# Kernel optimization log

Measured on AMD Instinct MI355X. Metric: run time of the kernel, lower is better.

## Reference

```python
import jax, jax.numpy as jnp
import numpy as np

N_HEAD, D_HEAD, EMBED = 16, 64, 1024
B, Q_LEN, MEM_LEN = 2, 1024, 1024
K_LEN = Q_LEN + MEM_LEN  # == r_len
LN_EPS = 1e-3  # keras LayerNormalization default


def rel_shift(x):
    # x: [B, H, q, r]  (Transformer-XL relative shift)
    b, h, q, r = x.shape
    x = jnp.pad(x, ((0, 0), (0, 0), (0, 0), (1, 0)))
    x = x.reshape(b, h, r + 1, q)[:, :, 1:, :]
    return x.reshape(b, h, q, r)


def setup_inputs() -> dict:
    key = jax.random.key(0)
    ks = jax.random.split(key, 12)
    s = 0.02
    w = jax.random.normal(ks[0], (B, Q_LEN, EMBED), jnp.float32)
    r = jax.random.normal(ks[1], (K_LEN, EMBED), jnp.float32)
    member = jax.random.normal(ks[2], (B, MEM_LEN, EMBED), jnp.float32)
    r_w_bias = jax.random.normal(ks[3], (N_HEAD, D_HEAD), jnp.float32) * s
    r_r_bias = jax.random.normal(ks[4], (N_HEAD, D_HEAD), jnp.float32) * s
    # causal mask over [q_len, k_len]: position i may attend to mem + keys <= mem_len+i
    qi = jnp.arange(Q_LEN)[:, None]
    kj = jnp.arange(K_LEN)[None, :]
    attn_mask = (kj > qi + MEM_LEN).astype(jnp.float32)
    Wq = jax.random.normal(ks[5], (EMBED, N_HEAD * D_HEAD), jnp.float32) * s
    Wk = jax.random.normal(ks[6], (EMBED, N_HEAD * D_HEAD), jnp.float32) * s
    Wv = jax.random.normal(ks[7], (EMBED, N_HEAD * D_HEAD), jnp.float32) * s
    Wr = jax.random.normal(ks[8], (EMBED, N_HEAD * D_HEAD), jnp.float32) * s
    Wo = jax.random.normal(ks[9], (N_HEAD * D_HEAD, EMBED), jnp.float32) * s
    ln_gamma = jnp.ones((EMBED,), jnp.float32)
    ln_beta = jnp.zeros((EMBED,), jnp.float32)
    return {"w": w, "r": r, "attn_mask": attn_mask, "r_w_bias": r_w_bias,
            "r_r_bias": r_r_bias, "member": member, "Wq": Wq, "Wk": Wk,
            "Wv": Wv, "Wr": Wr, "Wo": Wo, "ln_gamma": ln_gamma, "ln_beta": ln_beta}


def reference(w, r, attn_mask, r_w_bias, r_r_bias, member, Wq, Wk, Wv, Wr, Wo, ln_gamma, ln_beta):
    b, q_len, _ = w.shape
    cat = jnp.concatenate([member, w], axis=1)          # [B, klen, D]
    klen = cat.shape[1]
    q = (cat @ Wq)[:, -q_len:].reshape(b, q_len, N_HEAD, D_HEAD)
    k = (cat @ Wk).reshape(b, klen, N_HEAD, D_HEAD)
    v = (cat @ Wv).reshape(b, klen, N_HEAD, D_HEAD)
    rr = (r @ Wr).reshape(r.shape[0], N_HEAD, D_HEAD)    # [rlen, H, dh]
    rw_q = q + r_w_bias[None, None]                      # content bias
    rr_q = q + r_r_bias[None, None]                      # position bias
    AC = jnp.einsum('bqhd,bkhd->bhqk', rw_q, k)
    BD = jnp.einsum('bqhd,rhd->bhqr', rr_q, rr)
    BD = rel_shift(BD)
    attn = (AC + BD) / jnp.sqrt(jnp.float32(EMBED))      # note: sqrt(embed), as in source
    m = attn_mask[None, None]                            # [1,1,q,k]
    attn = attn * (1.0 - m) - 1e30 * m
    score = jax.nn.softmax(attn, axis=-1)
    out = jnp.einsum('bhqk,bkhd->bqhd', score, v).reshape(b, q_len, N_HEAD * D_HEAD)
    out = out @ Wo
    x = w + out
    mu = jnp.mean(x, axis=-1, keepdims=True)
    var = jnp.mean(jnp.square(x - mu), axis=-1, keepdims=True)
    return (x - mu) * jax.lax.rsqrt(var + LN_EPS) * ln_gamma + ln_beta
```

## Files before the change

kernel.cpp:

```cpp
#include <hip/hip_runtime.h>


typedef __bf16 bf16;
typedef __bf16 bf16x4 __attribute__((ext_vector_type(4)));
typedef __bf16 bf16x8 __attribute__((ext_vector_type(8)));
typedef float f32x4 __attribute__((ext_vector_type(4)));

#define MFMA16(a, b, c) __builtin_amdgcn_mfma_f32_16x16x32_bf16((a), (b), (c), 0, 0, 0)

constexpr int E = 1024;
constexpr int NH = 16;
constexpr int DH = 64;
constexpr int QL = 1024;
constexpr int ML = 1024;
constexpr int KLEN = 2048;

__device__ __forceinline__ void ldg2lds16(const bf16* g, bf16* l) {
    __builtin_amdgcn_global_load_lds(
        (const __attribute__((address_space(1))) unsigned int*)g,
        (__attribute__((address_space(3))) unsigned int*)l, 16, 0, 0);
}

__device__ __forceinline__ bf16x8 frag8(const bf16* t, int row, int ch) {
    return *(const bf16x8*)(t + row * 64 + ((ch ^ (row & 7)) << 3));
}

__global__ void pre_k(const float* __restrict__ Wq, const float* __restrict__ Wk,
                      const float* __restrict__ Wv, const float* __restrict__ Wr,
                      const float* __restrict__ Wo, const float* __restrict__ member,
                      const float* __restrict__ w, bf16* __restrict__ WqT,
                      bf16* __restrict__ WkT, bf16* __restrict__ WvT,
                      bf16* __restrict__ WrT, bf16* __restrict__ WoT,
                      bf16* __restrict__ cat) {
    const int id = blockIdx.x;
    const int tid = threadIdx.x;
    __shared__ float t[32][33];
    if (id < 5120) {
        const float* W; bf16* WT;
        switch (id >> 10) {
            case 0: W = Wq; WT = WqT; break;
            case 1: W = Wk; WT = WkT; break;
            case 2: W = Wv; WT = WvT; break;
            case 3: W = Wr; WT = WrT; break;
            default: W = Wo; WT = WoT; break;
        }
        int xy = id & 1023;
        int bx = (xy & 31) * 32, by = (xy >> 5) * 32;
        int x = tid & 31, y = tid >> 5;
        for (int yy = y; yy < 32; yy += 8)
            t[yy][x] = W[(by + yy) * E + bx + x];
        __syncthreads();
        for (int yy = y; yy < 32; yy += 8)
            WT[(bx + yy) * E + by + x] = (bf16)t[x][yy];
    } else {
        int row = id - 5120;
        int b = row >> 11, jj = row & 2047;
        const float* src = (jj < ML) ? member + ((size_t)(b * ML + jj)) * E
                                     : w + ((size_t)(b * QL + (jj - ML))) * E;
        float4 f = *(const float4*)(src + tid * 4);
        bf16x4 o;
        o[0] = (bf16)f.x; o[1] = (bf16)f.y; o[2] = (bf16)f.z; o[3] = (bf16)f.w;
        *(bf16x4*)(cat + (size_t)row * E + tid * 4) = o;
    }
}

__global__ __launch_bounds__(256) void proj_k(
    const bf16* __restrict__ cat, const float* __restrict__ r,
    const bf16* __restrict__ WqT, const bf16* __restrict__ WkT,
    const bf16* __restrict__ WvT, const bf16* __restrict__ WrT,
    const float* __restrict__ rwb, const float* __restrict__ rrb,
    bf16* __restrict__ Qw, bf16* __restrict__ Qr, bf16* __restrict__ Kh,
    bf16* __restrict__ Vt, bf16* __restrict__ RRh) {
    __shared__ __align__(16) bf16 As[128 * 64];
    __shared__ __align__(16) bf16 Bs[128 * 64];
    const int tid = threadIdx.x;
    const int wave = tid >> 6, lane = tid & 63, quad = lane >> 4, l16 = lane & 15;

    int id = blockIdx.x, zone, base;
    if (id < 128) { zone = 0; base = 0; }
    else if (id < 384) { zone = 1; base = 128; }
    else if (id < 640) { zone = 2; base = 384; }
    else { zone = 3; base = 640; }
    const int lid = id - base;
    const int bn = (lid & 7) * 128, bm = (lid >> 3) * 128;
    const bf16* Bt = (zone == 0) ? WqT : (zone == 1) ? WkT : (zone == 2) ? WvT : WrT;
    const int wm = (wave >> 1) * 64, wn = (wave & 1) * 64;

    f32x4 acc[4][4] = {};

    for (int kk = 0; kk < E; kk += 64) {
        if (zone == 3) {
            int srw = tid >> 3, cch = tid & 7;
            for (int c = 0; c < 4; ++c) {
                int row = c * 32 + srw;
                const float* ap = r + (size_t)(bm + row) * E + kk + cch * 8;
                float4 f0 = *(const float4*)ap;
                float4 f1 = *(const float4*)(ap + 4);
                bf16x8 v;
                v[0] = (bf16)f0.x; v[1] = (bf16)f0.y; v[2] = (bf16)f0.z; v[3] = (bf16)f0.w;
                v[4] = (bf16)f1.x; v[5] = (bf16)f1.y; v[6] = (bf16)f1.z; v[7] = (bf16)f1.w;
                *(bf16x8*)(As + row * 64 + ((cch ^ (row & 7)) << 3)) = v;
            }
        } else {
            for (int issue = 0; issue < 4; ++issue) {
                int q = (issue * 4 + wave) * 64 + lane;
                int row = q >> 3, cs = (q & 7) ^ ((q >> 3) & 7);
                int gm = bm + row;
                const bf16* ap;
                if (zone == 0) {
                    int b = gm >> 10;
                    ap = cat + ((size_t)(b * 2048 + 1024 + (gm & 1023))) * E;
                } else {
                    ap = cat + (size_t)gm * E;
                }
                ldg2lds16(ap + kk + cs * 8, As + (issue * 4 + wave) * 512);
            }
        }
        for (int issue = 0; issue < 4; ++issue) {
            int q = (issue * 4 + wave) * 64 + lane;
            int row = q >> 3, cs = (q & 7) ^ ((q >> 3) & 7);
            ldg2lds16(Bt + (size_t)(bn + row) * E + kk + cs * 8,
                      Bs + (issue * 4 + wave) * 512);
        }
        __syncthreads();
        for (int ks = 0; ks < 64; ks += 32) {
            bf16x8 af[4], bfr[4];
            for (int mt = 0; mt < 4; ++mt)
                af[mt] = frag8(As, wm + mt * 16 + l16, (ks >> 3) + quad);
            for (int nt = 0; nt < 4; ++nt)
                bfr[nt] = frag8(Bs, wn + nt * 16 + l16, (ks >> 3) + quad);
            for (int mt = 0; mt < 4; ++mt)
                for (int nt = 0; nt < 4; ++nt)
                    acc[mt][nt] = MFMA16(af[mt], bfr[nt], acc[mt][nt]);
        }
        __syncthreads();
    }

    if (zone == 2) {
        bf16* buf = ((wave < 2) ? As : Bs) + (wave & 1) * 4096;
        for (int mt = 0; mt < 4; ++mt)
            for (int nt = 0; nt < 4; ++nt)
                for (int rr = 0; rr < 4; ++rr) {
                    int lr = mt * 16 + quad * 4 + rr;
                    int lc = nt * 16 + l16;
                    buf[lr * 64 + (((lc >> 3) ^ (lr & 7)) << 3) + (lc & 7)] =
                        (bf16)acc[mt][nt][rr];
                }
        int h = (bn + wn) >> 6;
        int gmw = bm + wm;
        int b = gmw >> 11, jb = gmw & 2047;
        for (int dp = 0; dp < 8; ++dp) {
            int dl = dp * 8 + (lane >> 3);
            int jl = (lane & 7) * 8;
            bf16x8 tmp;
            for (int jj = 0; jj < 8; ++jj) {
                int rw = jl + jj;
                tmp[jj] = buf[rw * 64 + (((dl >> 3) ^ (rw & 7)) << 3) + (dl & 7)];
            }
            *(bf16x8*)(Vt + (((size_t)(b * NH + h) * DH + dl) * KLEN) + jb + jl) = tmp;
        }
        return;
    }

    for (int mt = 0; mt < 4; ++mt)
        for (int nt = 0; nt < 4; ++nt)
            for (int rr = 0; rr < 4; ++rr) {
                int row = bm + wm + mt * 16 + quad * 4 + rr;
                int col = bn + wn + nt * 16 + l16;
                float v = acc[mt][nt][rr];
                if (zone == 0) {
                    int b = row >> 10, i = row & 1023;
                    int h = col >> 6, d = col & 63;
                    size_t o = (((size_t)(b * NH + h) * QL) + i) * DH + d;
                    Qw[o] = (bf16)((v + rwb[col]) * 0.03125f);
                    Qr[o] = (bf16)((v + rrb[col]) * 0.03125f);
                } else if (zone == 1) {
                    int b = row >> 11, j = row & 2047;
                    int h = col >> 6, d = col & 63;
                    Kh[(((size_t)(b * NH + h) * KLEN) + j) * DH + d] = (bf16)v;
                } else {
                    int h = col >> 6, d = col & 63;
                    RRh[(((size_t)h * KLEN) + row) * DH + d] = (bf16)v;
                }
            }
}

__global__ __launch_bounds__(256) void attn_k(
    const bf16* __restrict__ Qw, const bf16* __restrict__ Qr,
    const bf16* __restrict__ Kh, const bf16* __restrict__ Vt,
    const bf16* __restrict__ RRh, bf16* __restrict__ AttO) {
    __shared__ __align__(16) bf16 Ks[2][64 * 64];
    __shared__ __align__(16) bf16 Vs[2][64 * 64];
    __shared__ __align__(16) bf16 RRing[3][64 * 64];
    __shared__ __align__(16) bf16 UB[4][16 * 88];

    const int tid = threadIdx.x;
    const int wave = tid >> 6, lane = tid & 63, quad = lane >> 4, l16 = lane & 15;
    const int id = blockIdx.x;
    const int b = id >> 8, h = (id >> 4) & 15;
    const int qt = (id < 256) ? (id & 15) : (15 - (id & 15));
    const int i0 = qt * 64;

    const bf16* Qwb = Qw + ((size_t)(b * NH + h) * QL) * DH;
    const bf16* Qrb = Qr + ((size_t)(b * NH + h) * QL) * DH;
    const bf16* Kb = Kh + ((size_t)(b * NH + h) * KLEN) * DH;
    const bf16* Vb = Vt + ((size_t)(b * NH + h) * DH) * KLEN;
    const bf16* Rb = RRh + ((size_t)h * KLEN) * DH;

    bf16x8 qw0, qw1, qr0, qr1;
    {
        int i = i0 + wave * 16 + l16;
        qw0 = *(const bf16x8*)(Qwb + (size_t)i * DH + quad * 8);
        qw1 = *(const bf16x8*)(Qwb + (size_t)i * DH + 32 + quad * 8);
        qr0 = *(const bf16x8*)(Qrb + (size_t)i * DH + quad * 8);
        qr1 = *(const bf16x8*)(Qrb + (size_t)i * DH + 32 + quad * 8);
    }

    float lpart[4] = {0.f, 0.f, 0.f, 0.f};
    f32x4 oacc[4] = {};

    const int ntiles = qt + 17;
    const int cbase = 15 - qt;
    const int ptbase = 3 - wave;

    auto stage_kv = [&](int t) {
        const int j0 = t * 64;
        bf16* Kd = Ks[t & 1];
        bf16* Vd = Vs[t & 1];
        for (int issue = 0; issue < 2; ++issue) {
            int q = (issue * 4 + wave) * 64 + lane;
            int row = q >> 3, cs = (q & 7) ^ ((q >> 3) & 7);
            ldg2lds16(Kb + (size_t)(j0 + row) * DH + cs * 8,
                      Kd + (issue * 4 + wave) * 512);
            ldg2lds16(Vb + (size_t)row * KLEN + j0 + cs * 8,
                      Vd + (issue * 4 + wave) * 512);
        }
    };
    auto stage_rr = [&](int c) {
        bf16* Rd = RRing[c % 3];
        for (int issue = 0; issue < 2; ++issue) {
            int q = (issue * 4 + wave) * 64 + lane;
            int row = q >> 3, cs = (q & 7) ^ ((q >> 3) & 7);
            int pr = c * 64 + row;
            pr = pr > KLEN - 1 ? KLEN - 1 : pr;
            ldg2lds16(Rb + (size_t)pr * DH + cs * 8, Rd + (issue * 4 + wave) * 512);
        }
    };

    stage_kv(0);
    stage_rr(cbase);
    stage_rr(cbase + 1);
    __syncthreads();

    for (int t = 0; t < ntiles; ++t) {
        const bf16* Kt = Ks[t & 1];
        const bf16* Vl = Vs[t & 1];
        const bf16* Rlo = RRing[(cbase + t) % 3];
        const bf16* Rhi = RRing[(cbase + t + 1) % 3];
        if (t + 1 < ntiles) {
            stage_kv(t + 1);
            stage_rr(cbase + t + 2);
        }

        f32x4 bacc[5];
        for (int pi = 0; pi < 5; ++pi) {
            int pt = ptbase + pi;
            const bf16* Rsrc = (pt < 4) ? Rlo : Rhi;
            int rrow = (pt & 3) * 16 + l16;
            f32x4 a = {};
            a = MFMA16(qr0, frag8(Rsrc, rrow, quad), a);
            a = MFMA16(qr1, frag8(Rsrc, rrow, 4 + quad), a);
            bacc[pi] = a;
        }

        f32x4 sacc[4];
        for (int nt = 0; nt < 4; ++nt) {
            f32x4 a = {};
            a = MFMA16(qw0, frag8(Kt, nt * 16 + l16, quad), a);
            a = MFMA16(qw1, frag8(Kt, nt * 16 + l16, 4 + quad), a);
            sacc[nt] = a;
        }

        float sv[4][4];
        const bool lastt = (t == ntiles - 1);
        for (int rr = 0; rr < 4; ++rr) {
            const int lr = quad * 4 + rr;
            const int srcl = quad * 16 + ((l16 - lr - 1) & 15);
            float g[5];
            for (int pi = 0; pi < 5; ++pi) g[pi] = __shfl(bacc[pi][rr], srcl);
            const bool hi = (l16 > lr);
            for (int nt = 0; nt < 4; ++nt) {
                float bdv = hi ? g[nt + 1] : g[nt];
                float p = __expf(sacc[nt][rr] + bdv);
                if (lastt) {
                    int i = i0 + wave * 16 + lr;
                    int j = t * 64 + nt * 16 + l16;
                    if (j > i + ML) p = 0.f;
                }
                sv[nt][rr] = p;
                lpart[rr] += p;
            }
        }

        for (int nt = 0; nt < 4; ++nt)
            for (int rr = 0; rr < 4; ++rr)
                UB[wave][(quad * 4 + rr) * 88 + nt * 16 + l16] = (bf16)sv[nt][rr];

        for (int c = 0; c < 2; ++c) {
            bf16x8 pa = *(const bf16x8*)(&UB[wave][l16 * 88 + c * 32 + quad * 8]);
            for (int nt = 0; nt < 4; ++nt) {
                bf16x8 vb = frag8(Vl, nt * 16 + l16, c * 4 + quad);
                oacc[nt] = MFMA16(pa, vb, oacc[nt]);
            }
        }
        __syncthreads();
    }

    float linv[4];
    for (int rr = 0; rr < 4; ++rr) {
        float v = lpart[rr];
        v += __shfl_xor(v, 1);
        v += __shfl_xor(v, 2);
        v += __shfl_xor(v, 4);
        v += __shfl_xor(v, 8);
        linv[rr] = 1.f / v;
    }

    for (int nt = 0; nt < 4; ++nt)
        for (int rr = 0; rr < 4; ++rr) {
            int i = i0 + wave * 16 + quad * 4 + rr;
            int d = nt * 16 + l16;
            AttO[((size_t)(b * QL + i)) * E + h * DH + d] =
                (bf16)(oacc[nt][rr] * linv[rr]);
        }
}

__global__ __launch_bounds__(256) void gemm_o(
    const bf16* __restrict__ A, const bf16* __restrict__ Bt,
    float* __restrict__ Xp) {
    __shared__ __align__(16) bf16 As[128 * 64];
    __shared__ __align__(16) bf16 Bs[128 * 64];
    const int tid = threadIdx.x;
    const int wave = tid >> 6, lane = tid & 63, quad = lane >> 4, l16 = lane & 15;
    const int bm = blockIdx.y * 128, bn = blockIdx.x * 128;
    const int kbase = blockIdx.z * 512;
    const int wm = (wave >> 1) * 64, wn = (wave & 1) * 64;

    f32x4 acc[4][4] = {};

    for (int s = 0; s < 8; ++s) {
        const int kk = kbase + s * 64;
        for (int issue = 0; issue < 4; ++issue) {
            int q = (issue * 4 + wave) * 64 + lane;
            int row = q >> 3, cs = (q & 7) ^ ((q >> 3) & 7);
            ldg2lds16(A + (size_t)(bm + row) * E + kk + cs * 8,
                      As + (issue * 4 + wave) * 512);
            ldg2lds16(Bt + (size_t)(bn + row) * E + kk + cs * 8,
                      Bs + (issue * 4 + wave) * 512);
        }
        __syncthreads();
        for (int ks = 0; ks < 64; ks += 32) {
            bf16x8 af[4], bfr[4];
            for (int mt = 0; mt < 4; ++mt)
                af[mt] = frag8(As, wm + mt * 16 + l16, (ks >> 3) + quad);
            for (int nt = 0; nt < 4; ++nt)
                bfr[nt] = frag8(Bs, wn + nt * 16 + l16, (ks >> 3) + quad);
            for (int mt = 0; mt < 4; ++mt)
                for (int nt = 0; nt < 4; ++nt)
                    acc[mt][nt] = MFMA16(af[mt], bfr[nt], acc[mt][nt]);
        }
        __syncthreads();
    }

    float* Xz = Xp + (size_t)blockIdx.z * 2048 * 1024;
    for (int mt = 0; mt < 4; ++mt)
        for (int nt = 0; nt < 4; ++nt)
            for (int rr = 0; rr < 4; ++rr) {
                int row = bm + wm + mt * 16 + quad * 4 + rr;
                int col = bn + wn + nt * 16 + l16;
                Xz[(size_t)row * E + col] = acc[mt][nt][rr];
            }
}

__global__ __launch_bounds__(256) void ln_k(const float* __restrict__ Xp,
                                            const float* __restrict__ resid,
                                            const float* __restrict__ gamma,
                                            const float* __restrict__ beta,
                                            float* __restrict__ out) {
    const int row = blockIdx.x;
    const int tid = threadIdx.x;
    const float* x0 = Xp + (size_t)row * E;
    const float* x1 = Xp + (size_t)2048 * 1024 + (size_t)row * E;
    const float* xr = resid + (size_t)row * E;
    float xv[4], s = 0.f, q = 0.f;
    for (int c = 0; c < 4; ++c) {
        int col = c * 256 + tid;
        float v = x0[col] + x1[col] + xr[col];
        xv[c] = v;
        s += v;
        q += v * v;
    }
    for (int off = 32; off > 0; off >>= 1) {
        s += __shfl_down(s, off);
        q += __shfl_down(q, off);
    }
    __shared__ float rs[4], rq[4];
    int wave = tid >> 6, lane = tid & 63;
    if (lane == 0) { rs[wave] = s; rq[wave] = q; }
    __syncthreads();
    float S = rs[0] + rs[1] + rs[2] + rs[3];
    float Q = rq[0] + rq[1] + rq[2] + rq[3];
    float mean = S * (1.f / E);
    float var = fmaxf(Q * (1.f / E) - mean * mean, 0.f);
    float rstd = rsqrtf(var + 1e-3f);
    for (int c = 0; c < 4; ++c) {
        int col = c * 256 + tid;
        out[(size_t)row * E + col] =
            (xv[c] - mean) * rstd * gamma[col] + beta[col];
    }
}

extern "C" void kernel_launch(void* const* d_in, const int* in_sizes, int n_in,
                              void* d_out, int out_size, void* d_ws,
                              size_t ws_size, hipStream_t stream) {
    (void)in_sizes; (void)n_in; (void)out_size; (void)ws_size;
    const float* w = (const float*)d_in[0];
    const float* r = (const float*)d_in[1];
    const float* rwb = (const float*)d_in[3];
    const float* rrb = (const float*)d_in[4];
    const float* member = (const float*)d_in[5];
    const float* Wq = (const float*)d_in[6];
    const float* Wk = (const float*)d_in[7];
    const float* Wv = (const float*)d_in[8];
    const float* Wr = (const float*)d_in[9];
    const float* Wo = (const float*)d_in[10];
    const float* gamma = (const float*)d_in[11];
    const float* beta = (const float*)d_in[12];
    float* out = (float*)d_out;

    char* ws = (char*)d_ws;
    const size_t MB = 1024 * 1024;
    bf16* WqT = (bf16*)(ws + 0 * MB);
    bf16* WkT = (bf16*)(ws + 2 * MB);
    bf16* WvT = (bf16*)(ws + 4 * MB);
    bf16* WrT = (bf16*)(ws + 6 * MB);
    bf16* WoT = (bf16*)(ws + 8 * MB);
    bf16* cat = (bf16*)(ws + 10 * MB);
    bf16* AttO = (bf16*)(ws + 14 * MB);
    bf16* Qw = (bf16*)(ws + 18 * MB);
    bf16* Qr = (bf16*)(ws + 22 * MB);
    float* Xp = (float*)(ws + 18 * MB);
    bf16* Kh = (bf16*)(ws + 26 * MB);
    bf16* Vt = (bf16*)(ws + 34 * MB);
    bf16* RRh = (bf16*)(ws + 42 * MB);

    pre_k<<<9216, 256, 0, stream>>>(Wq, Wk, Wv, Wr, Wo, member, w, WqT, WkT,
                                    WvT, WrT, WoT, cat);

    proj_k<<<768, 256, 0, stream>>>(cat, r, WqT, WkT, WvT, WrT, rwb, rrb, Qw,
                                    Qr, Kh, Vt, RRh);

    attn_k<<<512, 256, 0, stream>>>(Qw, Qr, Kh, Vt, RRh, AttO);

    gemm_o<<<dim3(8, 16, 2), 256, 0, stream>>>(AttO, WoT, Xp);
    ln_k<<<2048, 256, 0, stream>>>(Xp, w, gamma, beta, out);
}
```

Baseline: 257.8 us.

## Warp-specialize attention into score and PV waves with software pipelining

The attention kernel now launches 512 threads per block. Four waves compute the QK and positional scores plus the exponentials, and four other waves run the P·V MFMAs one tile behind, communicating through a double-buffered LDS probability buffer. The intent is to overlap the softmax/score phase with the PV matmul and to spread the staging loads across eight waves. It adds an extra pipeline iteration and raises register and LDS pressure per block, which may lower occupancy. Score waves pass the row normalizers to the PV waves through LDS at the end.

```diff
diff --git a/kernel.cpp b/kernel.cpp
--- a/kernel.cpp
+++ b/kernel.cpp
@@ -185,14 +185,14 @@
             }
 }
 
-__global__ __launch_bounds__(256) void attn_k(
+__global__ __launch_bounds__(512, 4) void attn_k(
     const bf16* __restrict__ Qw, const bf16* __restrict__ Qr,
     const bf16* __restrict__ Kh, const bf16* __restrict__ Vt,
     const bf16* __restrict__ RRh, bf16* __restrict__ AttO) {
     __shared__ __align__(16) bf16 Ks[2][64 * 64];
     __shared__ __align__(16) bf16 Vs[2][64 * 64];
     __shared__ __align__(16) bf16 RRing[3][64 * 64];
-    __shared__ __align__(16) bf16 UB[4][16 * 88];
+    __shared__ __align__(16) bf16 UB[2][4][16 * 88];
 
     const int tid = threadIdx.x;
     const int wave = tid >> 6, lane = tid & 63, quad = lane >> 4, l16 = lane & 15;
@@ -200,6 +200,8 @@
     const int b = id >> 8, h = (id >> 4) & 15;
     const int qt = (id < 256) ? (id & 15) : (15 - (id & 15));
     const int i0 = qt * 64;
+    const bool isS = wave < 4;
+    const int sw = isS ? wave : wave - 4;
 
     const bf16* Qwb = Qw + ((size_t)(b * NH + h) * QL) * DH;
     const bf16* Qrb = Qr + ((size_t)(b * NH + h) * QL) * DH;
@@ -208,8 +210,8 @@
     const bf16* Rb = RRh + ((size_t)h * KLEN) * DH;
 
     bf16x8 qw0, qw1, qr0, qr1;
-    {
-        int i = i0 + wave * 16 + l16;
+    if (isS) {
+        int i = i0 + sw * 16 + l16;
         qw0 = *(const bf16x8*)(Qwb + (size_t)i * DH + quad * 8);
         qw1 = *(const bf16x8*)(Qwb + (size_t)i * DH + 32 + quad * 8);
         qr0 = *(const bf16x8*)(Qrb + (size_t)i * DH + quad * 8);
@@ -221,118 +223,125 @@
 
     const int ntiles = qt + 17;
     const int cbase = 15 - qt;
-    const int ptbase = 3 - wave;
-
-    auto stage_kv = [&](int t) {
-        const int j0 = t * 64;
-        bf16* Kd = Ks[t & 1];
-        bf16* Vd = Vs[t & 1];
-        for (int issue = 0; issue < 2; ++issue) {
-            int q = (issue * 4 + wave) * 64 + lane;
-            int row = q >> 3, cs = (q & 7) ^ ((q >> 3) & 7);
-            ldg2lds16(Kb + (size_t)(j0 + row) * DH + cs * 8,
-                      Kd + (issue * 4 + wave) * 512);
-            ldg2lds16(Vb + (size_t)row * KLEN + j0 + cs * 8,
-                      Vd + (issue * 4 + wave) * 512);
-        }
+    const int ptbase = 3 - sw;
+
+    auto stageK = [&](int t) {
+        int q = wave * 64 + lane;
+        int row = q >> 3, cs = (q & 7) ^ (row & 7);
+        ldg2lds16(Kb + (size_t)(t * 64 + row) * DH + cs * 8,
+                  Ks[t & 1] + wave * 512);
     };
-    auto stage_rr = [&](int c) {
-        bf16* Rd = RRing[c % 3];
-        for (int issue = 0; issue < 2; ++issue) {
-            int q = (issue * 4 + wave) * 64 + lane;
-            int row = q >> 3, cs = (q & 7) ^ ((q >> 3) & 7);
-            int pr = c * 64 + row;
-            pr = pr > KLEN - 1 ? KLEN - 1 : pr;
-            ldg2lds16(Rb + (size_t)pr * DH + cs * 8, Rd + (issue * 4 + wave) * 512);
-        }
+    auto stageV = [&](int t) {
+        int q = wave * 64 + lane;
+        int row = q >> 3, cs = (q & 7) ^ (row & 7);
+        ldg2lds16(Vb + (size_t)row * KLEN + t * 64 + cs * 8,
+                  Vs[t & 1] + wave * 512);
     };
-
-    stage_kv(0);
-    stage_rr(cbase);
-    stage_rr(cbase + 1);
+    auto stageRR = [&](int c) {
+        int q = wave * 64 + lane;
+        int row = q >> 3, cs = (q & 7) ^ (row & 7);
+        int pr = c * 64 + row;
+        pr = pr > KLEN - 1 ? KLEN - 1 : pr;
+        ldg2lds16(Rb + (size_t)pr * DH + cs * 8, RRing[c % 3] + wave * 512);
+    };
+
+    stageK(0);
+    stageRR(cbase);
+    stageRR(cbase + 1);
     __syncthreads();
 
-    for (int t = 0; t < ntiles; ++t) {
-        const bf16* Kt = Ks[t & 1];
-        const bf16* Vl = Vs[t & 1];
-        const bf16* Rlo = RRing[(cbase + t) % 3];
-        const bf16* Rhi = RRing[(cbase + t + 1) % 3];
-        if (t + 1 < ntiles) {
-            stage_kv(t + 1);
-            stage_rr(cbase + t + 2);
-        }
-
-        f32x4 bacc[5];
-        for (int pi = 0; pi < 5; ++pi) {
-            int pt = ptbase + pi;
-            const bf16* Rsrc = (pt < 4) ? Rlo : Rhi;
-            int rrow = (pt & 3) * 16 + l16;
-            f32x4 a = {};
-            a = MFMA16(qr0, frag8(Rsrc, rrow, quad), a);
-            a = MFMA16(qr1, frag8(Rsrc, rrow, 4 + quad), a);
-            bacc[pi] = a;
-        }
-
-        f32x4 sacc[4];
-        for (int nt = 0; nt < 4; ++nt) {
-            f32x4 a = {};
-            a = MFMA16(qw0, frag8(Kt, nt * 16 + l16, quad), a);
-            a = MFMA16(qw1, frag8(Kt, nt * 16 + l16, 4 + quad), a);
-            sacc[nt] = a;
-        }
-
-        float sv[4][4];
-        const bool lastt = (t == ntiles - 1);
-        for (int rr = 0; rr < 4; ++rr) {
-            const int lr = quad * 4 + rr;
-            const int srcl = quad * 16 + ((l16 - lr - 1) & 15);
-            float g[5];
-            for (int pi = 0; pi < 5; ++pi) g[pi] = __shfl(bacc[pi][rr], srcl);
-            const bool hi = (l16 > lr);
-            for (int nt = 0; nt < 4; ++nt) {
-                float bdv = hi ? g[nt + 1] : g[nt];
-                float p = __expf(sacc[nt][rr] + bdv);
-                if (lastt) {
-                    int i = i0 + wave * 16 + lr;
-                    int j = t * 64 + nt * 16 + l16;
-                    if (j > i + ML) p = 0.f;
-                }
-                sv[nt][rr] = p;
-                lpart[rr] += p;
-            }
-        }
-
+    for (int p = 0; p <= ntiles; ++p) {
+        if (p + 1 < ntiles) {
+            stageK(p + 1);
+            stageRR(cbase + p + 2);
+        }
+        if (p < ntiles) stageV(p);
+
+        if (isS) {
+            if (p < ntiles) {
+                const bf16* Kt = Ks[p & 1];
+                const bf16* Rlo = RRing[(cbase + p) % 3];
+                const bf16* Rhi = RRing[(cbase + p + 1) % 3];
+
+                f32x4 bacc[5];
+                for (int pi = 0; pi < 5; ++pi) {
+                    int pt = ptbase + pi;
+                    const bf16* Rsrc = (pt < 4) ? Rlo : Rhi;
+                    int rrow = (pt & 3) * 16 + l16;
+                    f32x4 a = {};
+                    a = MFMA16(qr0, frag8(Rsrc, rrow, quad), a);
+                    a = MFMA16(qr1, frag8(Rsrc, rrow, 4 + quad), a);
+                    bacc[pi] = a;
+                }
+
+                f32x4 sacc[4];
+                for (int nt = 0; nt < 4; ++nt) {
+                    f32x4 a = {};
+                    a = MFMA16(qw0, frag8(Kt, nt * 16 + l16, quad), a);
+                    a = MFMA16(qw1, frag8(Kt, nt * 16 + l16, 4 + quad), a);
+                    sacc[nt] = a;
+                }
+
+                float sv[4][4];
+                const bool lastt = (p == ntiles - 1);
+                for (int rr = 0; rr < 4; ++rr) {
+                    const int lr = quad * 4 + rr;
+                    const int srcl = quad * 16 + ((l16 - lr - 1) & 15);
+                    float g[5];
+                    for (int pi = 0; pi < 5; ++pi) g[pi] = __shfl(bacc[pi][rr], srcl);
+                    const bool hi = (l16 > lr);
+                    for (int nt = 0; nt < 4; ++nt) {
+                        float bdv = hi ? g[nt + 1] : g[nt];
+                        float pv = __expf(sacc[nt][rr] + bdv);
+                        if (lastt) {
+                            int i = i0 + sw * 16 + lr;
+                            int j = p * 64 + nt * 16 + l16;
+                            if (j > i + ML) pv = 0.f;
+                        }
+                        sv[nt][rr] = pv;
+                        lpart[rr] += pv;
+                    }
+                }
+
+                bf16* UBd = UB[p & 1][sw];
+                for (int nt = 0; nt < 4; ++nt)
+                    for (int rr = 0; rr < 4; ++rr)
+                        UBd[(quad * 4 + rr) * 88 + nt * 16 + l16] = (bf16)sv[nt][rr];
+            } else {
+                float* lp = (float*)(&UB[ntiles & 1][sw][0]);
+                for (int rr = 0; rr < 4; ++rr) {
+                    float v = lpart[rr];
+                    v += __shfl_xor(v, 1);
+                    v += __shfl_xor(v, 2);
+                    v += __shfl_xor(v, 4);
+                    v += __shfl_xor(v, 8);
+                    lp[lane * 4 + rr] = 1.f / v;
+                }
+            }
+        } else if (p >= 1) {
+            const bf16* Vl = Vs[(p - 1) & 1];
+            const bf16* UBs = UB[(p - 1) & 1][sw];
+            for (int c = 0; c < 2; ++c) {
+                bf16x8 pa = *(const bf16x8*)(&UBs[l16 * 88 + c * 32 + quad * 8]);
+                for (int nt = 0; nt < 4; ++nt) {
+                    bf16x8 vb = frag8(Vl, nt * 16 + l16, c * 4 + quad);
+                    oacc[nt] = MFMA16(pa, vb, oacc[nt]);
+                }
+            }
+        }
+        __syncthreads();
+    }
+
+    if (!isS) {
+        const float* lp = (const float*)(&UB[ntiles & 1][sw][0]);
         for (int nt = 0; nt < 4; ++nt)
-            for (int rr = 0; rr < 4; ++rr)
-                UB[wave][(quad * 4 + rr) * 88 + nt * 16 + l16] = (bf16)sv[nt][rr];
-
-        for (int c = 0; c < 2; ++c) {
-            bf16x8 pa = *(const bf16x8*)(&UB[wave][l16 * 88 + c * 32 + quad * 8]);
-            for (int nt = 0; nt < 4; ++nt) {
-                bf16x8 vb = frag8(Vl, nt * 16 + l16, c * 4 + quad);
-                oacc[nt] = MFMA16(pa, vb, oacc[nt]);
-            }
-        }
-        __syncthreads();
-    }
-
-    float linv[4];
-    for (int rr = 0; rr < 4; ++rr) {
-        float v = lpart[rr];
-        v += __shfl_xor(v, 1);
-        v += __shfl_xor(v, 2);
-        v += __shfl_xor(v, 4);
-        v += __shfl_xor(v, 8);
-        linv[rr] = 1.f / v;
-    }
-
-    for (int nt = 0; nt < 4; ++nt)
-        for (int rr = 0; rr < 4; ++rr) {
-            int i = i0 + wave * 16 + quad * 4 + rr;
-            int d = nt * 16 + l16;
-            AttO[((size_t)(b * QL + i)) * E + h * DH + d] =
-                (bf16)(oacc[nt][rr] * linv[rr]);
-        }
+            for (int rr = 0; rr < 4; ++rr) {
+                int i = i0 + sw * 16 + quad * 4 + rr;
+                int d = nt * 16 + l16;
+                AttO[((size_t)(b * QL + i)) * E + h * DH + d] =
+                    (bf16)(oacc[nt][rr] * lp[lane * 4 + rr]);
+            }
+    }
 }
 
 __global__ __launch_bounds__(256) void gemm_o(
@@ -460,7 +469,7 @@
     proj_k<<<768, 256, 0, stream>>>(cat, r, WqT, WkT, WvT, WrT, rwb, rrb, Qw,
                                     Qr, Kh, Vt, RRh);
 
-    attn_k<<<512, 256, 0, stream>>>(Qw, Qr, Kh, Vt, RRh, AttO);
+    attn_k<<<512, 512, 0, stream>>>(Qw, Qr, Kh, Vt, RRh, AttO);
 
     gemm_o<<<dim3(8, 16, 2), 256, 0, stream>>>(AttO, WoT, Xp);
     ln_k<<<2048, 256, 0, stream>>>(Xp, w, gamma, beta, out);
```

Measured after the change: 251.1 us. 1.03x faster.
